# Kernel optimization log

Hardware: AMD Instinct MI355X
Metric: run time of the kernel (lower is better)

## Reference

```python
import jax, jax.numpy as jnp
import numpy as np

N = 50000      # nodes
E = 800000     # edges (avg degree 16)
IN = 256       # input feature dim
H = 128        # hidden dim
L = 2          # num layers
R = 8          # NUM_RELS_WITH_MASK
RD = 16        # rel_emb_dim
CONF_W = 0.5   # conf_log_weight
LN_EPS = 1e-5


def setup_inputs() -> dict:
    key = jax.random.key(0)
    ks = jax.random.split(key, 12)
    x = jax.random.normal(ks[0], (N, IN), dtype=jnp.float32)
    edge_index = jax.random.randint(ks[1], (2, E), 0, N, dtype=jnp.int32)
    edge_type = jax.random.randint(ks[2], (E,), 0, R, dtype=jnp.int32)
    edge_attr = jax.random.uniform(ks[3], (E, 1), dtype=jnp.float32)
    # encoder input projection (Linear with bias)
    W_in = jax.random.normal(ks[4], (IN, H), dtype=jnp.float32) / np.sqrt(IN)
    b_in = jnp.zeros((H,), dtype=jnp.float32)
    # per-layer params, stacked on leading L dim
    W_msg = jax.random.normal(ks[5], (L, H, H), dtype=jnp.float32) / np.sqrt(H)
    rel_emb = jax.random.normal(ks[6], (L, R, RD), dtype=jnp.float32)
    W_rel = jax.random.normal(ks[7], (L, RD, H), dtype=jnp.float32) / np.sqrt(RD)
    att_vec = jax.random.normal(ks[8], (L, 3 * H), dtype=jnp.float32) / np.sqrt(3 * H)
    bias = jnp.zeros((L, H), dtype=jnp.float32)
    ln_g = jnp.ones((L, H), dtype=jnp.float32)
    ln_b = jnp.zeros((L, H), dtype=jnp.float32)
    return {"x": x, "edge_index": edge_index, "edge_type": edge_type,
            "edge_attr": edge_attr, "W_in": W_in, "b_in": b_in,
            "W_msg": W_msg, "rel_emb": rel_emb, "W_rel": W_rel,
            "att_vec": att_vec, "bias": bias, "ln_g": ln_g, "ln_b": ln_b}


def _layer_norm(h, g, b):
    mu = jnp.mean(h, axis=-1, keepdims=True)
    var = jnp.mean(jnp.square(h - mu), axis=-1, keepdims=True)
    return (h - mu) * jax.lax.rsqrt(var + LN_EPS) * g + b


def reference(x, edge_index, edge_type, edge_attr,
              W_in, b_in, W_msg, rel_emb, W_rel, att_vec, bias, ln_g, ln_b):
    src, dst = edge_index[0], edge_index[1]
    t = jnp.clip(edge_type, 0, R - 1)
    log_conf = CONF_W * jnp.log(jnp.maximum(edge_attr[:, 0], 1e-6))  # [E]

    h = jax.nn.relu(x @ W_in + b_in)  # [N,H]
    for l in range(L):
        # project on nodes first (same math as projecting gathered rows, E >> N)
        hm = h @ W_msg[l]                 # [N,H]
        h_src = hm[src]                   # [E,H]
        h_dst = hm[dst]                   # [E,H]
        r = rel_emb[l][t] @ W_rel[l]      # [E,H]
        a = att_vec[l]
        a_d, a_s, a_r = a[:H], a[H:2 * H], a[2 * H:]
        e = h_dst @ a_d + h_src @ a_s + r @ a_r          # [E]
        e = jax.nn.leaky_relu(e, negative_slope=0.2) + log_conf
        # segment softmax grouped by dst
        m = jax.ops.segment_max(e, dst, num_segments=N)  # [N]
        ex = jnp.exp(e - m[dst])
        s = jax.ops.segment_sum(ex, dst, num_segments=N)  # [N]
        alpha = ex / s[dst]                               # [E]
        msg = h_src * alpha[:, None]                      # [E,H]
        out = jax.ops.segment_sum(msg, dst, num_segments=N) + bias[l]
        h = _layer_norm(h + jax.nn.relu(out), ln_g[l], ln_b[l])
    return h
```

## Files before the change

### kernel.cpp

```cpp
#include <hip/hip_runtime.h>
#include <hip/hip_bf16.h>

#define N_NODES 50000
#define NE      800000
#define IN_DIM  256
#define H_DIM   128
#define NL      2
#define NR      8
#define RD_DIM  16
#define CONF_W  0.5f
#define LN_EPS  1e-5f

#define SCAN_CHUNK 1024
#define NB_SCAN    ((N_NODES + SCAN_CHUNK - 1) / SCAN_CHUNK)
#define DCAP       128

typedef __attribute__((ext_vector_type(8))) short bf16x8;
typedef __attribute__((ext_vector_type(4))) float f32x4;

__device__ __forceinline__ unsigned short f2bf(float f) {
    unsigned u = __float_as_uint(f);
    u += 0x7fffu + ((u >> 16) & 1u);
    return (unsigned short)(u >> 16);
}
__device__ __forceinline__ float bf2f(unsigned short v) {
    return __uint_as_float(((unsigned)v) << 16);
}


__global__ void k_zero_counts(int* __restrict__ counts) {
    int i = blockIdx.x * 256 + threadIdx.x;
    if (i < N_NODES) counts[i] = 0;
}

__global__ void k_count(const int* __restrict__ dstv, int* __restrict__ counts,
                        int* __restrict__ rank) {
    int i = blockIdx.x * 256 + threadIdx.x;
    if (i >= NE) return;
    rank[i] = atomicAdd(counts + dstv[i], 1);
}

__global__ __launch_bounds__(256) void k_scan1(const int* __restrict__ counts,
                                               int* __restrict__ bsum) {
    __shared__ int lsum[256];
    const int t = threadIdx.x, b = blockIdx.x;
    const int base = b * SCAN_CHUNK + t * 4;
    int s = 0;
#pragma unroll
    for (int j = 0; j < 4; ++j) {
        int idx = base + j;
        if (idx < N_NODES) s += counts[idx];
    }
    lsum[t] = s;
    __syncthreads();
    for (int off = 128; off; off >>= 1) {
        if (t < off) lsum[t] += lsum[t + off];
        __syncthreads();
    }
    if (t == 0) bsum[b] = lsum[0];
}

__global__ void k_scan2(const int* __restrict__ bsum, int* __restrict__ bbase) {
    int lane = threadIdx.x & 63;
    int v = (lane < NB_SCAN) ? bsum[lane] : 0;
    int inc = v;
    for (int off = 1; off < 64; off <<= 1) {
        int tmp = __shfl_up(inc, off);
        if (lane >= off) inc += tmp;
    }
    if (lane < NB_SCAN) bbase[lane] = inc - v;
}

__global__ __launch_bounds__(256) void k_scan3(const int* __restrict__ counts,
                                               const int* __restrict__ bbase,
                                               int* __restrict__ offsets) {
    __shared__ int lsum[256];
    const int t = threadIdx.x, b = blockIdx.x;
    const int base = b * SCAN_CHUNK + t * 4;
    int c[4];
    int s = 0;
#pragma unroll
    for (int j = 0; j < 4; ++j) {
        int idx = base + j;
        c[j] = (idx < N_NODES) ? counts[idx] : 0;
        s += c[j];
    }
    lsum[t] = s;
    __syncthreads();
    for (int off = 1; off < 256; off <<= 1) {
        int v = (t >= off) ? lsum[t - off] : 0;
        __syncthreads();
        lsum[t] += v;
        __syncthreads();
    }
    int run = bbase[b] + lsum[t] - s;
#pragma unroll
    for (int j = 0; j < 4; ++j) {
        int idx = base + j;
        if (idx < N_NODES) { offsets[idx] = run; run += c[j]; }
    }
}

__global__ void k_perm(const int* __restrict__ srcv, const int* __restrict__ dstv,
                       const int* __restrict__ et, const float* __restrict__ ea,
                       const int* __restrict__ offsets, const int* __restrict__ rank,
                       uint2* __restrict__ meta_sorted) {
    int i = blockIdx.x * 256 + threadIdx.x;
    if (i >= NE) return;
    int p = offsets[dstv[i]] + rank[i];
    int t = et[i]; t = t < 0 ? 0 : (t > NR - 1 ? NR - 1 : t);
    float lc = CONF_W * logf(fmaxf(ea[i], 1e-6f));
    meta_sorted[p] = make_uint2((unsigned)srcv[i] | ((unsigned)t << 16),
                                __float_as_uint(lc));
}

__global__ void k_rel_score(const float* __restrict__ rel_emb,
                            const float* __restrict__ W_rel,
                            const float* __restrict__ att_vec,
                            float* __restrict__ rel_score) {
    __shared__ float wvec[NL][RD_DIM];
    int t = threadIdx.x;
    if (t < NL * RD_DIM) {
        int l = t / RD_DIM, d = t % RD_DIM;
        const float* wr = W_rel + ((size_t)l * RD_DIM + d) * H_DIM;
        const float* ar = att_vec + (size_t)l * 3 * H_DIM + 2 * H_DIM;
        float s = 0.f;
        for (int k = 0; k < H_DIM; ++k) s += wr[k] * ar[k];
        wvec[l][d] = s;
    }
    __syncthreads();
    if (t < NL * NR) {
        int l = t / NR, r = t % NR;
        const float* re = rel_emb + ((size_t)l * NR + r) * RD_DIM;
        float s = 0.f;
        for (int d = 0; d < RD_DIM; ++d) s += re[d] * wvec[l][d];
        rel_score[t] = s;
    }
}

__global__ void k_cvt_weights(const float* __restrict__ W_in,
                              const float* __restrict__ W_msg,
                              unsigned short* __restrict__ Wt_in,
                              unsigned short* __restrict__ Wt_msg) {
    int i = blockIdx.x * 256 + threadIdx.x;
    if (i < H_DIM * IN_DIM) {
        int n = i >> 8, k = i & 255;
        Wt_in[i] = f2bf(W_in[(size_t)k * H_DIM + n]);
    } else if (i < H_DIM * IN_DIM + NL * H_DIM * H_DIM) {
        int r = i - H_DIM * IN_DIM;
        int l = r >> 14;
        int n = (r >> 7) & 127, k = r & 127;
        Wt_msg[r] = f2bf(W_msg[(size_t)l * H_DIM * H_DIM + (size_t)k * H_DIM + n]);
    }
}

__global__ void k_zero_scores(float* __restrict__ dsc, float* __restrict__ ssc) {
    int i = blockIdx.x * 256 + threadIdx.x;
    if (i < NL * N_NODES) { dsc[i] = 0.f; ssc[i] = 0.f; }
}

template <int K, bool ABF16, bool BIASRELU, bool SCORES>
__global__ __launch_bounds__(256) void k_gemm_mfma(
        const void* __restrict__ Av, const unsigned short* __restrict__ Bt,
        const float* __restrict__ bias, float* __restrict__ Cf,
        unsigned short* __restrict__ Cb, int M,
        const float* __restrict__ att_vec_l,
        float* __restrict__ dsc, float* __restrict__ ssc) {
    __shared__ unsigned short As[128 * 40];
    __shared__ unsigned short Bs[128 * 40];
    const int t = threadIdx.x;
    const int wid = t >> 6, lane = t & 63;
    const int wr = wid >> 1, wc = wid & 1;
    const int lm = lane & 15, lg = lane >> 4;
    const int m0 = blockIdx.x * 128;

    f32x4 acc[4][4] = {};

    for (int k0 = 0; k0 < K; k0 += 32) {
        if (ABF16) {
            const unsigned short* A = (const unsigned short*)Av;
#pragma unroll
            for (int i = 0; i < 2; ++i) {
                int flat = t + i * 256;
                int row = flat >> 2, ch = flat & 3;
                int rm = m0 + row; rm = rm < M ? rm : M - 1;
                uint4 v = *(const uint4*)(A + (size_t)rm * K + k0 + ch * 8);
                *(uint4*)(As + row * 40 + ch * 8) = v;
            }
        } else {
            const float* A = (const float*)Av;
#pragma unroll
            for (int i = 0; i < 4; ++i) {
                int flat = t + i * 256;
                int row = flat >> 3, c4 = flat & 7;
                int rm = m0 + row; rm = rm < M ? rm : M - 1;
                float4 fv = *(const float4*)(A + (size_t)rm * K + k0 + c4 * 4);
                uint2 pk;
                pk.x = (unsigned)f2bf(fv.x) | ((unsigned)f2bf(fv.y) << 16);
                pk.y = (unsigned)f2bf(fv.z) | ((unsigned)f2bf(fv.w) << 16);
                *(uint2*)(As + row * 40 + c4 * 4) = pk;
            }
        }
#pragma unroll
        for (int i = 0; i < 2; ++i) {
            int flat = t + i * 256;
            int row = flat >> 2, ch = flat & 3;
            uint4 v = *(const uint4*)(Bt + (size_t)row * K + k0 + ch * 8);
            *(uint4*)(Bs + row * 40 + ch * 8) = v;
        }
        __syncthreads();
        bf16x8 a[4], b[4];
#pragma unroll
        for (int f = 0; f < 4; ++f) {
            a[f] = *(const bf16x8*)(As + (wr * 64 + f * 16 + lm) * 40 + lg * 8);
            b[f] = *(const bf16x8*)(Bs + (wc * 64 + f * 16 + lm) * 40 + lg * 8);
        }
#pragma unroll
        for (int fm = 0; fm < 4; ++fm)
#pragma unroll
            for (int fn = 0; fn < 4; ++fn)
                acc[fm][fn] = __builtin_amdgcn_mfma_f32_16x16x32_bf16(
                    a[fm], b[fn], acc[fm][fn], 0, 0, 0);
        __syncthreads();
    }

    float av[4], asv[4];
    if (SCORES) {
#pragma unroll
        for (int fn = 0; fn < 4; ++fn) {
            int n = wc * 64 + fn * 16 + lm;
            av[fn]  = att_vec_l[n];
            asv[fn] = att_vec_l[H_DIM + n];
        }
    }

#pragma unroll
    for (int fm = 0; fm < 4; ++fm) {
#pragma unroll
        for (int j = 0; j < 4; ++j) {
            int m = m0 + wr * 64 + fm * 16 + lg * 4 + j;
            bool valid = m < M;
            if (BIASRELU) {
#pragma unroll
                for (int fn = 0; fn < 4; ++fn) {
                    int n = wc * 64 + fn * 16 + lm;
                    float v = fmaxf(acc[fm][fn][j] + bias[n], 0.f);
                    if (valid) {
                        Cf[(size_t)m * H_DIM + n] = v;
                        if (Cb) Cb[(size_t)m * H_DIM + n] = f2bf(v);
                    }
                }
            }
            if (SCORES) {
                float pd = 0.f, ps = 0.f;
#pragma unroll
                for (int fn = 0; fn < 4; ++fn) {
                    int n = wc * 64 + fn * 16 + lm;
                    float v = acc[fm][fn][j];
                    if (valid) Cb[(size_t)m * H_DIM + n] = f2bf(v);
                    pd += v * av[fn];
                    ps += v * asv[fn];
                }
#pragma unroll
                for (int off = 8; off; off >>= 1) {
                    pd += __shfl_xor(pd, off);
                    ps += __shfl_xor(ps, off);
                }
                if (lm == 0 && valid) {
                    atomicAdd(dsc + m, pd);
                    atomicAdd(ssc + m, ps);
                }
            }
        }
    }
}

__global__ __launch_bounds__(256) void k_fused(
        const int* __restrict__ offsets, const int* __restrict__ counts,
        const uint2* __restrict__ meta,
        const float* __restrict__ dsc, const float* __restrict__ ssc,
        const float* __restrict__ rel_l,
        const unsigned short* __restrict__ hm, const float* __restrict__ h_in,
        const float* __restrict__ bias_l, const float* __restrict__ g,
        const float* __restrict__ b, float* __restrict__ h_out,
        unsigned short* __restrict__ h_out_bf) {
    __shared__ float rel_s[NR];
    __shared__ float es[4][DCAP];
    __shared__ unsigned short srcs[4][DCAP];
    if (threadIdx.x < NR) rel_s[threadIdx.x] = rel_l[threadIdx.x];
    __syncthreads();

    const int wave = threadIdx.x >> 6, lane = threadIdx.x & 63;
    const int d = blockIdx.x * 4 + wave;

    const int start = offsets[d];
    const int deg = counts[d];
    const float dsc_d = dsc[d];

    float m_l = -1e30f;
    for (int j = lane; j < deg; j += 64) {
        uint2 mv = meta[start + j];
        int s = mv.x & 0xffff;
        float e = dsc_d + ssc[s] + rel_s[(mv.x >> 16) & 7];
        e = (e > 0.f ? e : 0.2f * e) + __uint_as_float(mv.y);
        if (j < DCAP) { es[wave][j] = e; srcs[wave][j] = (unsigned short)s; }
        m_l = fmaxf(m_l, e);
    }
    float m = m_l;
    for (int off = 32; off; off >>= 1) m = fmaxf(m, __shfl_xor(m, off));

    float s_l = 0.f;
    for (int j = lane; j < deg; j += 64) {
        float e;
        if (j < DCAP) e = es[wave][j];
        else {
            uint2 mv = meta[start + j];
            e = dsc_d + ssc[mv.x & 0xffff] + rel_s[(mv.x >> 16) & 7];
            e = (e > 0.f ? e : 0.2f * e) + __uint_as_float(mv.y);
        }
        float w = __expf(e - m);
        if (j < DCAP) es[wave][j] = w;
        s_l += w;
    }
    float ssum = s_l;
    for (int off = 32; off; off >>= 1) ssum += __shfl_xor(ssum, off);

    __syncthreads();

    float2 acc = make_float2(0.f, 0.f);
    const int c = 2 * lane;
#pragma unroll 4
    for (int k = 0; k < deg; ++k) {
        float w;
        int s;
        if (k < DCAP) { w = es[wave][k]; s = srcs[wave][k]; }
        else {
            uint2 mv = meta[start + k];
            s = mv.x & 0xffff;
            float e = dsc_d + ssc[s] + rel_s[(mv.x >> 16) & 7];
            e = (e > 0.f ? e : 0.2f * e) + __uint_as_float(mv.y);
            w = __expf(e - m);
        }
        ushort2 rv = *(const ushort2*)(hm + (size_t)s * H_DIM + c);
        acc.x += w * bf2f(rv.x);
        acc.y += w * bf2f(rv.y);
    }

    const float inv = (deg > 0) ? 1.f / ssum : 0.f;
    float2 bs = *(const float2*)(bias_l + c);
    float2 hi = *(const float2*)(h_in + (size_t)d * H_DIM + c);
    float v0 = hi.x + fmaxf(acc.x * inv + bs.x, 0.f);
    float v1 = hi.y + fmaxf(acc.y * inv + bs.y, 0.f);

    float sum = v0 + v1;
    for (int off = 32; off; off >>= 1) sum += __shfl_xor(sum, off);
    float mu = sum * (1.f / H_DIM);
    float d0 = v0 - mu, d1 = v1 - mu;
    float vs = d0 * d0 + d1 * d1;
    for (int off = 32; off; off >>= 1) vs += __shfl_xor(vs, off);
    float invstd = rsqrtf(vs * (1.f / H_DIM) + LN_EPS);
    float2 gg = *(const float2*)(g + c);
    float2 bb = *(const float2*)(b + c);
    float2 o;
    o.x = d0 * invstd * gg.x + bb.x;
    o.y = d1 * invstd * gg.y + bb.y;
    *(float2*)(h_out + (size_t)d * H_DIM + c) = o;
    if (h_out_bf) {
        ushort2 ob = make_ushort2(f2bf(o.x), f2bf(o.y));
        *(ushort2*)(h_out_bf + (size_t)d * H_DIM + c) = ob;
    }
}

extern "C" void kernel_launch(void* const* d_in, const int* in_sizes, int n_in,
                              void* d_out, int out_size, void* d_ws, size_t ws_size,
                              hipStream_t stream) {
    const float* x         = (const float*)d_in[0];
    const int*   edge_index= (const int*)d_in[1];
    const int*   edge_type = (const int*)d_in[2];
    const float* edge_attr = (const float*)d_in[3];
    const float* W_in      = (const float*)d_in[4];
    const float* b_in      = (const float*)d_in[5];
    const float* W_msg     = (const float*)d_in[6];
    const float* rel_emb   = (const float*)d_in[7];
    const float* W_rel     = (const float*)d_in[8];
    const float* att_vec   = (const float*)d_in[9];
    const float* bias      = (const float*)d_in[10];
    const float* ln_g      = (const float*)d_in[11];
    const float* ln_b      = (const float*)d_in[12];
    float* out = (float*)d_out;

    char* w = (char*)d_ws;
    float* h_ws       = (float*)w; w += (size_t)N_NODES * H_DIM * 4;
    unsigned short* h_bf = (unsigned short*)w; w += (size_t)N_NODES * H_DIM * 2;
    unsigned short* hm_b = (unsigned short*)w; w += (size_t)N_NODES * H_DIM * 2;
    uint2* meta_sorted = (uint2*)w; w += (size_t)NE * 8;
    int*   rank       = (int*)w;   w += (size_t)NE * 4;
    int*   counts     = (int*)w;   w += (size_t)N_NODES * 4;
    int*   offsets    = (int*)w;   w += (size_t)N_NODES * 4;
    float* dsc        = (float*)w; w += (size_t)NL * N_NODES * 4;
    float* ssc        = (float*)w; w += (size_t)NL * N_NODES * 4;
    unsigned short* Wt_in  = (unsigned short*)w; w += (size_t)H_DIM * IN_DIM * 2;
    unsigned short* Wt_msg = (unsigned short*)w; w += (size_t)NL * H_DIM * H_DIM * 2;
    float* rel_score  = (float*)w; w += 64 * 4;
    int*   bsum       = (int*)w;   w += 64 * 4;
    int*   bbase      = (int*)w;   w += 64 * 4;

    const int* srcv = edge_index;
    const int* dstv = edge_index + NE;

    k_zero_counts<<<(N_NODES + 255) / 256, 256, 0, stream>>>(counts);
    k_count<<<(NE + 255) / 256, 256, 0, stream>>>(dstv, counts, rank);
    k_scan1<<<NB_SCAN, 256, 0, stream>>>(counts, bsum);
    k_scan2<<<1, 64, 0, stream>>>(bsum, bbase);
    k_scan3<<<NB_SCAN, 256, 0, stream>>>(counts, bbase, offsets);
    k_perm<<<(NE + 255) / 256, 256, 0, stream>>>(srcv, dstv, edge_type, edge_attr,
                                                 offsets, rank, meta_sorted);
    k_rel_score<<<1, 256, 0, stream>>>(rel_emb, W_rel, att_vec, rel_score);
    k_cvt_weights<<<(H_DIM * IN_DIM + NL * H_DIM * H_DIM + 255) / 256, 256, 0, stream>>>(
        W_in, W_msg, Wt_in, Wt_msg);
    k_zero_scores<<<(NL * N_NODES + 255) / 256, 256, 0, stream>>>(dsc, ssc);

    const int GB = (N_NODES + 127) / 128;
    k_gemm_mfma<IN_DIM, false, true, false><<<GB, 256, 0, stream>>>(
        x, Wt_in, b_in, h_ws, h_bf, N_NODES, nullptr, nullptr, nullptr);

    for (int l = 0; l < NL; ++l) {
        k_gemm_mfma<H_DIM, true, false, true><<<GB, 256, 0, stream>>>(
            h_bf, Wt_msg + (size_t)l * H_DIM * H_DIM, nullptr, nullptr, hm_b, N_NODES,
            att_vec + (size_t)l * 3 * H_DIM, dsc + (size_t)l * N_NODES,
            ssc + (size_t)l * N_NODES);
        k_fused<<<N_NODES / 4, 256, 0, stream>>>(
            offsets, counts, meta_sorted,
            dsc + (size_t)l * N_NODES, ssc + (size_t)l * N_NODES,
            rel_score + l * NR, hm_b, h_ws,
            bias + (size_t)l * H_DIM, ln_g + (size_t)l * H_DIM,
            ln_b + (size_t)l * H_DIM,
            (l == NL - 1) ? out : h_ws,
            (l == NL - 1) ? nullptr : h_bf);
    }
}
```

Baseline: 329.8 us.

## Vectorize neighbor gather with 16-lane groups and drop fp32 residual buffer

The aggregation kernel now assigns each 16-lane group to a different edge. Each lane loads 8 bf16 features with one 16-byte load, and partial sums are reduced across groups with shuffles. The separate exp-sum pass is folded into the aggregation loop. The fp32 hidden-state buffer is removed, so the residual is read from the bf16 copy, and weight conversion and score zeroing share one launch. This aims to raise memory-level parallelism in the gather and cut global traffic and launches, at the cost of lower residual precision and redundant LayerNorm work across the four groups.

New measurement: 309.7 us. -6.1%, faster.

```diff
diff --git a/kernel.cpp b/kernel.cpp
--- a/kernel.cpp
+++ b/kernel.cpp
@@ -23,8 +23,11 @@
     u += 0x7fffu + ((u >> 16) & 1u);
     return (unsigned short)(u >> 16);
 }
-__device__ __forceinline__ float bf2f(unsigned short v) {
-    return __uint_as_float(((unsigned)v) << 16);
+__device__ __forceinline__ float bf_lo(unsigned v) {
+    return __uint_as_float(v << 16);
+}
+__device__ __forceinline__ float bf_hi(unsigned v) {
+    return __uint_as_float(v & 0xffff0000u);
 }
 
 
@@ -138,10 +141,11 @@
     }
 }
 
-__global__ void k_cvt_weights(const float* __restrict__ W_in,
-                              const float* __restrict__ W_msg,
-                              unsigned short* __restrict__ Wt_in,
-                              unsigned short* __restrict__ Wt_msg) {
+__global__ void k_setup(const float* __restrict__ W_in,
+                        const float* __restrict__ W_msg,
+                        unsigned short* __restrict__ Wt_in,
+                        unsigned short* __restrict__ Wt_msg,
+                        float* __restrict__ dsc, float* __restrict__ ssc) {
     int i = blockIdx.x * 256 + threadIdx.x;
     if (i < H_DIM * IN_DIM) {
         int n = i >> 8, k = i & 255;
@@ -152,17 +156,13 @@
         int n = (r >> 7) & 127, k = r & 127;
         Wt_msg[r] = f2bf(W_msg[(size_t)l * H_DIM * H_DIM + (size_t)k * H_DIM + n]);
     }
-}
-
-__global__ void k_zero_scores(float* __restrict__ dsc, float* __restrict__ ssc) {
-    int i = blockIdx.x * 256 + threadIdx.x;
     if (i < NL * N_NODES) { dsc[i] = 0.f; ssc[i] = 0.f; }
 }
 
 template <int K, bool ABF16, bool BIASRELU, bool SCORES>
 __global__ __launch_bounds__(256) void k_gemm_mfma(
         const void* __restrict__ Av, const unsigned short* __restrict__ Bt,
-        const float* __restrict__ bias, float* __restrict__ Cf,
+        const float* __restrict__ bias,
         unsigned short* __restrict__ Cb, int M,
         const float* __restrict__ att_vec_l,
         float* __restrict__ dsc, float* __restrict__ ssc) {
@@ -245,10 +245,7 @@
                 for (int fn = 0; fn < 4; ++fn) {
                     int n = wc * 64 + fn * 16 + lm;
                     float v = fmaxf(acc[fm][fn][j] + bias[n], 0.f);
-                    if (valid) {
-                        Cf[(size_t)m * H_DIM + n] = v;
-                        if (Cb) Cb[(size_t)m * H_DIM + n] = f2bf(v);
-                    }
+                    if (valid) Cb[(size_t)m * H_DIM + n] = f2bf(v);
                 }
             }
             if (SCORES) {
@@ -280,10 +277,11 @@
         const uint2* __restrict__ meta,
         const float* __restrict__ dsc, const float* __restrict__ ssc,
         const float* __restrict__ rel_l,
-        const unsigned short* __restrict__ hm, const float* __restrict__ h_in,
+        const unsigned short* __restrict__ hm,
+        const unsigned short* __restrict__ h_in_bf,
         const float* __restrict__ bias_l, const float* __restrict__ g,
-        const float* __restrict__ b, float* __restrict__ h_out,
-        unsigned short* __restrict__ h_out_bf) {
+        const float* __restrict__ b,
+        float* __restrict__ h_out_f32, unsigned short* __restrict__ h_out_bf) {
     __shared__ float rel_s[NR];
     __shared__ float es[4][DCAP];
     __shared__ unsigned short srcs[4][DCAP];
@@ -291,6 +289,7 @@
     __syncthreads();
 
     const int wave = threadIdx.x >> 6, lane = threadIdx.x & 63;
+    const int sub = lane & 15, grp = lane >> 4;
     const int d = blockIdx.x * 4 + wave;
 
     const int start = offsets[d];
@@ -309,65 +308,94 @@
     float m = m_l;
     for (int off = 32; off; off >>= 1) m = fmaxf(m, __shfl_xor(m, off));
 
-    float s_l = 0.f;
-    for (int j = lane; j < deg; j += 64) {
-        float e;
-        if (j < DCAP) e = es[wave][j];
-        else {
-            uint2 mv = meta[start + j];
-            e = dsc_d + ssc[mv.x & 0xffff] + rel_s[(mv.x >> 16) & 7];
-            e = (e > 0.f ? e : 0.2f * e) + __uint_as_float(mv.y);
-        }
-        float w = __expf(e - m);
-        if (j < DCAP) es[wave][j] = w;
-        s_l += w;
-    }
-    float ssum = s_l;
-    for (int off = 32; off; off >>= 1) ssum += __shfl_xor(ssum, off);
-
     __syncthreads();
 
-    float2 acc = make_float2(0.f, 0.f);
-    const int c = 2 * lane;
-#pragma unroll 4
-    for (int k = 0; k < deg; ++k) {
-        float w;
-        int s;
-        if (k < DCAP) { w = es[wave][k]; s = srcs[wave][k]; }
-        else {
-            uint2 mv = meta[start + k];
-            s = mv.x & 0xffff;
-            float e = dsc_d + ssc[s] + rel_s[(mv.x >> 16) & 7];
-            e = (e > 0.f ? e : 0.2f * e) + __uint_as_float(mv.y);
-            w = __expf(e - m);
-        }
-        ushort2 rv = *(const ushort2*)(hm + (size_t)s * H_DIM + c);
-        acc.x += w * bf2f(rv.x);
-        acc.y += w * bf2f(rv.y);
-    }
-
-    const float inv = (deg > 0) ? 1.f / ssum : 0.f;
-    float2 bs = *(const float2*)(bias_l + c);
-    float2 hi = *(const float2*)(h_in + (size_t)d * H_DIM + c);
-    float v0 = hi.x + fmaxf(acc.x * inv + bs.x, 0.f);
-    float v1 = hi.y + fmaxf(acc.y * inv + bs.y, 0.f);
-
-    float sum = v0 + v1;
+    float a0 = 0.f, a1 = 0.f, a2 = 0.f, a3 = 0.f,
+          a4 = 0.f, a5 = 0.f, a6 = 0.f, a7 = 0.f;
+    float s_part = 0.f;
+#pragma unroll 2
+    for (int k0 = 0; k0 < deg; k0 += 4) {
+        int k = k0 + grp;
+        if (k < deg) {
+            float e; int s;
+            if (k < DCAP) { e = es[wave][k]; s = srcs[wave][k]; }
+            else {
+                uint2 mv = meta[start + k];
+                s = mv.x & 0xffff;
+                e = dsc_d + ssc[s] + rel_s[(mv.x >> 16) & 7];
+                e = (e > 0.f ? e : 0.2f * e) + __uint_as_float(mv.y);
+            }
+            float w = __expf(e - m);
+            s_part += w;
+            uint4 rv = *(const uint4*)(hm + (size_t)s * H_DIM + sub * 8);
+            a0 += w * bf_lo(rv.x); a1 += w * bf_hi(rv.x);
+            a2 += w * bf_lo(rv.y); a3 += w * bf_hi(rv.y);
+            a4 += w * bf_lo(rv.z); a5 += w * bf_hi(rv.z);
+            a6 += w * bf_lo(rv.w); a7 += w * bf_hi(rv.w);
+        }
+    }
+    a0 += __shfl_xor(a0, 16); a1 += __shfl_xor(a1, 16);
+    a2 += __shfl_xor(a2, 16); a3 += __shfl_xor(a3, 16);
+    a4 += __shfl_xor(a4, 16); a5 += __shfl_xor(a5, 16);
+    a6 += __shfl_xor(a6, 16); a7 += __shfl_xor(a7, 16);
+    s_part += __shfl_xor(s_part, 16);
+    a0 += __shfl_xor(a0, 32); a1 += __shfl_xor(a1, 32);
+    a2 += __shfl_xor(a2, 32); a3 += __shfl_xor(a3, 32);
+    a4 += __shfl_xor(a4, 32); a5 += __shfl_xor(a5, 32);
+    a6 += __shfl_xor(a6, 32); a7 += __shfl_xor(a7, 32);
+    s_part += __shfl_xor(s_part, 32);
+
+    const float inv = (deg > 0) ? 1.f / s_part : 0.f;
+
+    uint4 hv = *(const uint4*)(h_in_bf + (size_t)d * H_DIM + sub * 8);
+    float4 b0 = *(const float4*)(bias_l + sub * 8);
+    float4 b1 = *(const float4*)(bias_l + sub * 8 + 4);
+    float v0 = bf_lo(hv.x) + fmaxf(a0 * inv + b0.x, 0.f);
+    float v1 = bf_hi(hv.x) + fmaxf(a1 * inv + b0.y, 0.f);
+    float v2 = bf_lo(hv.y) + fmaxf(a2 * inv + b0.z, 0.f);
+    float v3 = bf_hi(hv.y) + fmaxf(a3 * inv + b0.w, 0.f);
+    float v4 = bf_lo(hv.z) + fmaxf(a4 * inv + b1.x, 0.f);
+    float v5 = bf_hi(hv.z) + fmaxf(a5 * inv + b1.y, 0.f);
+    float v6 = bf_lo(hv.w) + fmaxf(a6 * inv + b1.z, 0.f);
+    float v7 = bf_hi(hv.w) + fmaxf(a7 * inv + b1.w, 0.f);
+
+    float sum = v0 + v1 + v2 + v3 + v4 + v5 + v6 + v7;
     for (int off = 32; off; off >>= 1) sum += __shfl_xor(sum, off);
-    float mu = sum * (1.f / H_DIM);
-    float d0 = v0 - mu, d1 = v1 - mu;
-    float vs = d0 * d0 + d1 * d1;
+    float mu = sum * (1.f / (H_DIM * 4));
+    float d0 = v0 - mu, d1 = v1 - mu, d2 = v2 - mu, d3 = v3 - mu;
+    float d4 = v4 - mu, d5 = v5 - mu, d6 = v6 - mu, d7 = v7 - mu;
+    float vs = d0 * d0 + d1 * d1 + d2 * d2 + d3 * d3 +
+               d4 * d4 + d5 * d5 + d6 * d6 + d7 * d7;
     for (int off = 32; off; off >>= 1) vs += __shfl_xor(vs, off);
-    float invstd = rsqrtf(vs * (1.f / H_DIM) + LN_EPS);
-    float2 gg = *(const float2*)(g + c);
-    float2 bb = *(const float2*)(b + c);
-    float2 o;
-    o.x = d0 * invstd * gg.x + bb.x;
-    o.y = d1 * invstd * gg.y + bb.y;
-    *(float2*)(h_out + (size_t)d * H_DIM + c) = o;
-    if (h_out_bf) {
-        ushort2 ob = make_ushort2(f2bf(o.x), f2bf(o.y));
-        *(ushort2*)(h_out_bf + (size_t)d * H_DIM + c) = ob;
+    float invstd = rsqrtf(vs * (1.f / (H_DIM * 4)) + LN_EPS);
+
+    float4 g0 = *(const float4*)(g + sub * 8);
+    float4 g1 = *(const float4*)(g + sub * 8 + 4);
+    float4 bb0 = *(const float4*)(b + sub * 8);
+    float4 bb1 = *(const float4*)(b + sub * 8 + 4);
+    float o0 = d0 * invstd * g0.x + bb0.x;
+    float o1 = d1 * invstd * g0.y + bb0.y;
+    float o2 = d2 * invstd * g0.z + bb0.z;
+    float o3 = d3 * invstd * g0.w + bb0.w;
+    float o4 = d4 * invstd * g1.x + bb1.x;
+    float o5 = d5 * invstd * g1.y + bb1.y;
+    float o6 = d6 * invstd * g1.z + bb1.z;
+    float o7 = d7 * invstd * g1.w + bb1.w;
+
+    if (grp == 0) {
+        if (h_out_f32) {
+            float* p = h_out_f32 + (size_t)d * H_DIM + sub * 8;
+            *(float4*)p = make_float4(o0, o1, o2, o3);
+            *(float4*)(p + 4) = make_float4(o4, o5, o6, o7);
+        }
+        if (h_out_bf) {
+            uint4 pk;
+            pk.x = (unsigned)f2bf(o0) | ((unsigned)f2bf(o1) << 16);
+            pk.y = (unsigned)f2bf(o2) | ((unsigned)f2bf(o3) << 16);
+            pk.z = (unsigned)f2bf(o4) | ((unsigned)f2bf(o5) << 16);
+            pk.w = (unsigned)f2bf(o6) | ((unsigned)f2bf(o7) << 16);
+            *(uint4*)(h_out_bf + (size_t)d * H_DIM + sub * 8) = pk;
+        }
     }
 }
 
@@ -390,7 +418,6 @@
     float* out = (float*)d_out;
 
     char* w = (char*)d_ws;
-    float* h_ws       = (float*)w; w += (size_t)N_NODES * H_DIM * 4;
     unsigned short* h_bf = (unsigned short*)w; w += (size_t)N_NODES * H_DIM * 2;
     unsigned short* hm_b = (unsigned short*)w; w += (size_t)N_NODES * H_DIM * 2;
     uint2* meta_sorted = (uint2*)w; w += (size_t)NE * 8;
@@ -416,26 +443,25 @@
     k_perm<<<(NE + 255) / 256, 256, 0, stream>>>(srcv, dstv, edge_type, edge_attr,
                                                  offsets, rank, meta_sorted);
     k_rel_score<<<1, 256, 0, stream>>>(rel_emb, W_rel, att_vec, rel_score);
-    k_cvt_weights<<<(H_DIM * IN_DIM + NL * H_DIM * H_DIM + 255) / 256, 256, 0, stream>>>(
-        W_in, W_msg, Wt_in, Wt_msg);
-    k_zero_scores<<<(NL * N_NODES + 255) / 256, 256, 0, stream>>>(dsc, ssc);
+    k_setup<<<(NL * N_NODES + 255) / 256, 256, 0, stream>>>(
+        W_in, W_msg, Wt_in, Wt_msg, dsc, ssc);
 
     const int GB = (N_NODES + 127) / 128;
     k_gemm_mfma<IN_DIM, false, true, false><<<GB, 256, 0, stream>>>(
-        x, Wt_in, b_in, h_ws, h_bf, N_NODES, nullptr, nullptr, nullptr);
+        x, Wt_in, b_in, h_bf, N_NODES, nullptr, nullptr, nullptr);
 
     for (int l = 0; l < NL; ++l) {
         k_gemm_mfma<H_DIM, true, false, true><<<GB, 256, 0, stream>>>(
-            h_bf, Wt_msg + (size_t)l * H_DIM * H_DIM, nullptr, nullptr, hm_b, N_NODES,
+            h_bf, Wt_msg + (size_t)l * H_DIM * H_DIM, nullptr, hm_b, N_NODES,
             att_vec + (size_t)l * 3 * H_DIM, dsc + (size_t)l * N_NODES,
             ssc + (size_t)l * N_NODES);
         k_fused<<<N_NODES / 4, 256, 0, stream>>>(
             offsets, counts, meta_sorted,
             dsc + (size_t)l * N_NODES, ssc + (size_t)l * N_NODES,
-            rel_score + l * NR, hm_b, h_ws,
+            rel_score + l * NR, hm_b, h_bf,
             bias + (size_t)l * H_DIM, ln_g + (size_t)l * H_DIM,
             ln_b + (size_t)l * H_DIM,
-            (l == NL - 1) ? out : h_ws,
+            (l == NL - 1) ? out : nullptr,
             (l == NL - 1) ? nullptr : h_bf);
     }
 }
```
